# Optimization experiments

Hardware: AMD Instinct MI355X
Metric: run time of the kernel (lower is better)

## Reference

```python
import jax, jax.numpy as jnp
import numpy as np

B, H, W, C = 8, 64, 64, 256
NUM_HEADS = 8
HEAD_DIM = C // NUM_HEADS
H_SP, W_SP = 64, 8  # idx=0: h_sp=H, w_sp=split_size[1]
SCALE = HEAD_DIM ** -0.5


def img2windows(img):
    # img: [B, C, H, W] -> [B*nW, h_sp*w_sp, C]
    b, c, h, w = img.shape
    x = img.reshape(b, c, h // H_SP, H_SP, w // W_SP, W_SP)
    x = jnp.transpose(x, (0, 2, 4, 3, 5, 1))
    return x.reshape(-1, H_SP * W_SP, c)


def im2cswin(x):
    # x: [B, L, C] -> [B*nW, heads, h_sp*w_sp, head_dim]
    xi = jnp.transpose(x, (0, 2, 1)).reshape(B, C, H, W)
    xw = img2windows(xi)
    xw = xw.reshape(-1, H_SP * W_SP, NUM_HEADS, HEAD_DIM)
    return jnp.transpose(xw, (0, 2, 1, 3))


def get_lepe(x, conv_w, conv_b):
    xi = jnp.transpose(x, (0, 2, 1)).reshape(B, C, H, W)
    xi = xi.reshape(B, C, H // H_SP, H_SP, W // W_SP, W_SP)
    xi = jnp.transpose(xi, (0, 2, 4, 1, 3, 5)).reshape(-1, C, H_SP, W_SP)
    # depthwise 3x3 conv, padding 1
    lepe = jax.lax.conv_general_dilated(
        xi, conv_w, window_strides=(1, 1), padding=((1, 1), (1, 1)),
        feature_group_count=C, dimension_numbers=('NCHW', 'OIHW', 'NCHW'))
    lepe = lepe + conv_b[None, :, None, None]
    def to_heads(t):
        t = t.reshape(-1, NUM_HEADS, HEAD_DIM, H_SP * W_SP)
        return jnp.transpose(t, (0, 1, 3, 2))
    return to_heads(xi), to_heads(lepe)


def windows2img(xw):
    # xw: [B*nW, h_sp*w_sp, C] -> [B, H, W, C]
    x = xw.reshape(B, H // H_SP, W // W_SP, H_SP, W_SP, C)
    x = jnp.transpose(x, (0, 1, 3, 2, 4, 5))
    return x.reshape(B, H, W, C)


def setup_inputs() -> dict:
    key = jax.random.key(0)
    k1, k2, k3 = jax.random.split(key, 3)
    x = jax.random.normal(k1, (3, B, H * W, C), dtype=jnp.float32)
    conv_w = jax.random.normal(k2, (C, 1, 3, 3), dtype=jnp.float32) * 0.1
    conv_b = jax.random.normal(k3, (C,), dtype=jnp.float32) * 0.1
    return {"x": x, "conv_w": conv_w, "conv_b": conv_b}


def reference(x, conv_w, conv_b):
    q, k, v = x[0], x[1], x[2]
    qh = im2cswin(q) * SCALE          # [nW*B, h, S, d]
    kh = im2cswin(k)
    vh, lepe = get_lepe(v, conv_w, conv_b)
    attn = jnp.einsum('whsd,whtd->whst', qh, kh)
    attn = jax.nn.softmax(attn, axis=-1)
    out = jnp.einsum('whst,whtd->whsd', attn, vh) + lepe
    out = jnp.transpose(out, (0, 2, 1, 3)).reshape(-1, H_SP * W_SP, C)
    return windows2img(out).reshape(B, H * W, C)
```

## Files before the change

kernel.cpp:

```cpp
#include <hip/hip_runtime.h>

typedef __attribute__((ext_vector_type(8))) __bf16 bf16x8;
typedef __attribute__((ext_vector_type(4))) __bf16 bf16x4;
typedef __attribute__((ext_vector_type(4))) _Float16 half4;
typedef __attribute__((ext_vector_type(4))) float floatx4;

static __device__ __forceinline__ floatx4 mfma_qk(bf16x8 a, bf16x8 b, floatx4 c) {
    return __builtin_amdgcn_mfma_f32_16x16x32_bf16(a, b, c, 0, 0, 0);
}
static __device__ __forceinline__ floatx4 mfma_pv(half4 a, half4 b, floatx4 c) {
    return __builtin_amdgcn_mfma_f32_16x16x16f16(a, b, c, 0, 0, 0);
}

static __device__ __forceinline__ float4 gload4(const float* p) {
    float4 r;
    asm volatile("global_load_dwordx4 %0, %1, off"
                 : "=v"(r) : "v"(p) : "memory");
    return r;
}

#define QSCALE 0.25504099302278787f

__global__ __launch_bounds__(256, 2) void lepe_attn_kernel(
    const float* __restrict__ x, const float* __restrict__ conv_w,
    const float* __restrict__ conv_b, float* __restrict__ out)
{
    const int bx = blockIdx.x;
    const int wi = bx >> 4;
    const int hd = (bx >> 1) & 7;
    const int shalf = bx & 1;
    const int b = wi >> 3, wblk = wi & 7;
    const int tid = threadIdx.x;
    const int wave = tid >> 6, lane = tid & 63;
    const int g = lane >> 4, ln = lane & 15;

    __shared__ __align__(16) __bf16   Ks[2][128][32];
    __shared__ __align__(16) _Float16 VsT[32][522];
    __shared__ float Wc[32][9];
    __shared__ float Bc[32];

    const float* qp = x;
    const float* kp = x + 8 * 4096 * 256;
    const float* vp = x + 2 * 8 * 4096 * 256;
    const int base  = b * 4096 * 256;
    const int cbase = hd * 32;
    const int wcol0 = wblk * 8;
    const int qcb   = shalf * 8 + wave;

    int tP[4], fP[4], off0[4];
    #pragma unroll
    for (int p = 0; p < 4; p++) {
        int i = tid + p * 256;
        tP[p] = i >> 3; fP[p] = i & 7;
        off0[p] = base + ((tP[p] >> 3) << 14) + (wcol0 + (tP[p] & 7)) * 256
                + cbase + fP[p] * 4;
    }

    float4 kx[4], vx[4];
    #pragma unroll
    for (int p = 0; p < 4; p++) {
        kx[p] = gload4(kp + off0[p]);
        vx[p] = gload4(vp + off0[p]);
    }

    bf16x8 bq[4];
    #pragma unroll
    for (int c = 0; c < 2; c++) {
        #pragma unroll
        for (int ss = 0; ss < 2; ss++) {
            int s = (qcb + 4 * c) * 32 + ss * 16 + ln;
            int l = ((s >> 3) << 6) + wcol0 + (s & 7);
            const float* qb = qp + base + l * 256 + cbase + g * 8;
            float4 a = *(const float4*)qb, d = *(const float4*)(qb + 4);
            bf16x8 q;
            q[0] = (__bf16)(a.x * QSCALE); q[1] = (__bf16)(a.y * QSCALE);
            q[2] = (__bf16)(a.z * QSCALE); q[3] = (__bf16)(a.w * QSCALE);
            q[4] = (__bf16)(d.x * QSCALE); q[5] = (__bf16)(d.y * QSCALE);
            q[6] = (__bf16)(d.z * QSCALE); q[7] = (__bf16)(d.w * QSCALE);
            bq[c * 2 + ss] = q;
        }
    }

    asm volatile("s_waitcnt vmcnt(0)" ::: "memory");
    __builtin_amdgcn_sched_barrier(0);
    #pragma unroll
    for (int p = 0; p < 4; p++) {
        bf16x4 kk = { (__bf16)kx[p].x, (__bf16)kx[p].y,
                      (__bf16)kx[p].z, (__bf16)kx[p].w };
        *(bf16x4*)&Ks[0][tP[p]][fP[p] * 4] = kk;
        VsT[fP[p]*4+0][tP[p]] = (_Float16)vx[p].x;
        VsT[fP[p]*4+1][tP[p]] = (_Float16)vx[p].y;
        VsT[fP[p]*4+2][tP[p]] = (_Float16)vx[p].z;
        VsT[fP[p]*4+3][tP[p]] = (_Float16)vx[p].w;
    }
    for (int i = tid; i < 288; i += 256)
        Wc[i / 9][i % 9] = conv_w[(cbase + i / 9) * 9 + (i % 9)];
    if (tid < 32) Bc[tid] = conv_b[cbase + tid];
    __syncthreads();

    floatx4 aLo[4], aHi[4], aSum[4];
    #pragma unroll
    for (int u = 0; u < 4; u++) {
        aLo[u]  = (floatx4){0.f,0.f,0.f,0.f};
        aHi[u]  = (floatx4){0.f,0.f,0.f,0.f};
        aSum[u] = (floatx4){0.f,0.f,0.f,0.f};
    }
    const floatx4 zf = {0.f,0.f,0.f,0.f};
    const half4 ones = {(_Float16)1.f,(_Float16)1.f,(_Float16)1.f,(_Float16)1.f};

    auto compute_tile = [&](int j) {
        const __bf16 (*KT)[32] = Ks[j & 1];
        #pragma unroll 4
        for (int tl = 0; tl < 8; tl++) {
            bf16x8 ak = *(const bf16x8*)&KT[tl * 16 + ln][g * 8];
            int tcol = j * 128 + tl * 16 + g * 4;
            const unsigned* r0 = (const unsigned*)&VsT[ln][0];
            const unsigned* r1 = (const unsigned*)&VsT[16 + ln][0];
            half4 av0, av1;
            ((unsigned*)&av0)[0] = r0[tcol >> 1];
            ((unsigned*)&av0)[1] = r0[(tcol >> 1) + 1];
            ((unsigned*)&av1)[0] = r1[tcol >> 1];
            ((unsigned*)&av1)[1] = r1[(tcol >> 1) + 1];
            #pragma unroll
            for (int u = 0; u < 4; u++) {
                floatx4 sc = mfma_qk(ak, bq[u], zf);
                half4 ph;
                #pragma unroll
                for (int r = 0; r < 4; r++)
                    ph[r] = (_Float16)__builtin_amdgcn_exp2f(sc[r]);
                aLo[u]  = mfma_pv(av0, ph, aLo[u]);
                aHi[u]  = mfma_pv(av1, ph, aHi[u]);
                aSum[u] = mfma_pv(ones, ph, aSum[u]);
            }
        }
    };

    for (int j = 0; j < 3; j++) {
        #pragma unroll
        for (int p = 0; p < 4; p++) {
            const float* kq = kp + off0[p] + (j + 1) * 262144;
            const float* vq = vp + off0[p] + (j + 1) * 262144;
            kx[p] = gload4(kq);
            vx[p] = gload4(vq);
        }

        __builtin_amdgcn_s_setprio(1);
        compute_tile(j);
        __builtin_amdgcn_s_setprio(0);

        asm volatile("s_waitcnt vmcnt(0)" ::: "memory");
        __builtin_amdgcn_sched_barrier(0);
        #pragma unroll
        for (int p = 0; p < 4; p++) {
            bf16x4 kk = { (__bf16)kx[p].x, (__bf16)kx[p].y,
                          (__bf16)kx[p].z, (__bf16)kx[p].w };
            *(bf16x4*)&Ks[(j + 1) & 1][tP[p]][fP[p] * 4] = kk;
            int tg = 128 * (j + 1) + tP[p];
            VsT[fP[p]*4+0][tg] = (_Float16)vx[p].x;
            VsT[fP[p]*4+1][tg] = (_Float16)vx[p].y;
            VsT[fP[p]*4+2][tg] = (_Float16)vx[p].z;
            VsT[fP[p]*4+3][tg] = (_Float16)vx[p].w;
        }
        __syncthreads();
    }
    __builtin_amdgcn_s_setprio(1);
    compute_tile(3);
    __builtin_amdgcn_s_setprio(0);

    float inv[4];
    #pragma unroll
    for (int u = 0; u < 4; u++)
        inv[u] = 1.0f / aSum[u][0];

    #pragma unroll
    for (int c = 0; c < 2; c++) {
        #pragma unroll
        for (int ss = 0; ss < 2; ss++) {
            int u = c * 2 + ss;
            int s = (qcb + 4 * c) * 32 + ss * 16 + ln;
            int h = s >> 3, w = s & 7;
            int l = h * 64 + wcol0 + w;
            floatx4 alo = aLo[u], ahi = aHi[u];
            float4 olo, ohi;
            #pragma unroll
            for (int r = 0; r < 4; r++) {
                int ddl = g * 4 + r;
                float lepl = Bc[ddl];
                float leph = Bc[16 + ddl];
                #pragma unroll
                for (int ky = 0; ky < 3; ky++) {
                    int hh = h + ky - 1;
                    bool okh = (hh >= 0) & (hh < 64);
                    #pragma unroll
                    for (int kx2 = 0; kx2 < 3; kx2++) {
                        int ww = w + kx2 - 1;
                        bool ok = okh & (ww >= 0) & (ww < 8);
                        float vl = ok ? (float)VsT[ddl][hh * 8 + ww] : 0.f;
                        float vh = ok ? (float)VsT[16 + ddl][hh * 8 + ww] : 0.f;
                        lepl = fmaf(vl, Wc[ddl][ky * 3 + kx2], lepl);
                        leph = fmaf(vh, Wc[16 + ddl][ky * 3 + kx2], leph);
                    }
                }
                ((float*)&olo)[r] = alo[r] * inv[u] + lepl;
                ((float*)&ohi)[r] = ahi[r] * inv[u] + leph;
            }
            float* ob = out + base + l * 256 + cbase;
            *(float4*)(ob + g * 4) = olo;
            *(float4*)(ob + 16 + g * 4) = ohi;
        }
    }
}

extern "C" void kernel_launch(void* const* d_in, const int* in_sizes, int n_in,
                              void* d_out, int out_size, void* d_ws, size_t ws_size,
                              hipStream_t stream) {
    const float* x  = (const float*)d_in[0];
    const float* cw = (const float*)d_in[1];
    const float* cb = (const float*)d_in[2];
    float* out = (float*)d_out;
    lepe_attn_kernel<<<dim3(1024), dim3(256), 0, stream>>>(x, cw, cb, out);
}
```

Measured before the change: 192.8 us.

## Process full window per block and load all K/V up front

Each block now handles all 512 queries of a window-head instead of half, so the grid drops from 1024 to 512 blocks and each K/V tile is staged once per window-head rather than twice. The double-buffered per-tile K/V pipeline is replaced by issuing all 32 global loads at once and draining them in order with staged vmcnt waits into a single full-size K buffer, followed by one compute loop. This halves redundant K/V global traffic and conversion work but doubles accumulator and Q registers per thread and removes load/compute overlap, which can hurt occupancy under launch_bounds(256,2). With only 512 blocks, device fill may also suffer.

Result: no change. 196.3 us (+1.8%).

```diff
diff --git a/kernel.cpp b/kernel.cpp
--- a/kernel.cpp
+++ b/kernel.cpp
@@ -26,15 +26,13 @@
     const float* __restrict__ conv_b, float* __restrict__ out)
 {
     const int bx = blockIdx.x;
-    const int wi = bx >> 4;
-    const int hd = (bx >> 1) & 7;
-    const int shalf = bx & 1;
+    const int wi = bx >> 3, hd = bx & 7;
     const int b = wi >> 3, wblk = wi & 7;
     const int tid = threadIdx.x;
     const int wave = tid >> 6, lane = tid & 63;
     const int g = lane >> 4, ln = lane & 15;
 
-    __shared__ __align__(16) __bf16   Ks[2][128][32];
+    __shared__ __align__(16) __bf16   Ks[512][32];
     __shared__ __align__(16) _Float16 VsT[32][522];
     __shared__ float Wc[32][9];
     __shared__ float Bc[32];
@@ -45,30 +43,17 @@
     const int base  = b * 4096 * 256;
     const int cbase = hd * 32;
     const int wcol0 = wblk * 8;
-    const int qcb   = shalf * 8 + wave;
 
-    int tP[4], fP[4], off0[4];
+    const int f  = tid & 7, t0 = tid >> 3;
+    const int off0 = base + (((t0 >> 3) << 6) + wcol0 + (t0 & 7)) * 256
+                   + cbase + f * 4;
+
+    bf16x8 bq[8];
     #pragma unroll
-    for (int p = 0; p < 4; p++) {
-        int i = tid + p * 256;
-        tP[p] = i >> 3; fP[p] = i & 7;
-        off0[p] = base + ((tP[p] >> 3) << 14) + (wcol0 + (tP[p] & 7)) * 256
-                + cbase + fP[p] * 4;
-    }
-
-    float4 kx[4], vx[4];
-    #pragma unroll
-    for (int p = 0; p < 4; p++) {
-        kx[p] = gload4(kp + off0[p]);
-        vx[p] = gload4(vp + off0[p]);
-    }
-
-    bf16x8 bq[4];
-    #pragma unroll
-    for (int c = 0; c < 2; c++) {
+    for (int c = 0; c < 4; c++) {
         #pragma unroll
         for (int ss = 0; ss < 2; ss++) {
-            int s = (qcb + 4 * c) * 32 + ss * 16 + ln;
+            int s = (wave + 4 * c) * 32 + ss * 16 + ln;
             int l = ((s >> 3) << 6) + wcol0 + (s & 7);
             const float* qb = qp + base + l * 256 + cbase + g * 8;
             float4 a = *(const float4*)qb, d = *(const float4*)(qb + 4);
@@ -81,26 +66,43 @@
         }
     }
 
-    asm volatile("s_waitcnt vmcnt(0)" ::: "memory");
-    __builtin_amdgcn_sched_barrier(0);
-    #pragma unroll
-    for (int p = 0; p < 4; p++) {
-        bf16x4 kk = { (__bf16)kx[p].x, (__bf16)kx[p].y,
-                      (__bf16)kx[p].z, (__bf16)kx[p].w };
-        *(bf16x4*)&Ks[0][tP[p]][fP[p] * 4] = kk;
-        VsT[fP[p]*4+0][tP[p]] = (_Float16)vx[p].x;
-        VsT[fP[p]*4+1][tP[p]] = (_Float16)vx[p].y;
-        VsT[fP[p]*4+2][tP[p]] = (_Float16)vx[p].z;
-        VsT[fP[p]*4+3][tP[p]] = (_Float16)vx[p].w;
-    }
     for (int i = tid; i < 288; i += 256)
         Wc[i / 9][i % 9] = conv_w[(cbase + i / 9) * 9 + (i % 9)];
     if (tid < 32) Bc[tid] = conv_b[cbase + tid];
+
+    __builtin_amdgcn_sched_barrier(0);
+
+    float4 kx[16], vx[16];
+    #pragma unroll
+    for (int it = 0; it < 16; it++) {
+        kx[it] = gload4(kp + off0 + it * 65536);
+        vx[it] = gload4(vp + off0 + it * 65536);
+    }
+
+#define DRAIN_PAIR(IT, CNT) do {                                           \
+        asm volatile("s_waitcnt vmcnt(" #CNT ")" ::: "memory");            \
+        __builtin_amdgcn_sched_barrier(0);                                 \
+        int t = t0 + (IT) * 32;                                            \
+        bf16x4 kk = { (__bf16)kx[IT].x, (__bf16)kx[IT].y,                  \
+                      (__bf16)kx[IT].z, (__bf16)kx[IT].w };                \
+        *(bf16x4*)&Ks[t][f * 4] = kk;                                      \
+        VsT[f*4+0][t] = (_Float16)vx[IT].x;                                \
+        VsT[f*4+1][t] = (_Float16)vx[IT].y;                                \
+        VsT[f*4+2][t] = (_Float16)vx[IT].z;                                \
+        VsT[f*4+3][t] = (_Float16)vx[IT].w;                                \
+    } while (0)
+
+    DRAIN_PAIR(0, 30);  DRAIN_PAIR(1, 28);  DRAIN_PAIR(2, 26);  DRAIN_PAIR(3, 24);
+    DRAIN_PAIR(4, 22);  DRAIN_PAIR(5, 20);  DRAIN_PAIR(6, 18);  DRAIN_PAIR(7, 16);
+    DRAIN_PAIR(8, 14);  DRAIN_PAIR(9, 12);  DRAIN_PAIR(10, 10); DRAIN_PAIR(11, 8);
+    DRAIN_PAIR(12, 6);  DRAIN_PAIR(13, 4);  DRAIN_PAIR(14, 2);  DRAIN_PAIR(15, 0);
+#undef DRAIN_PAIR
+
     __syncthreads();
 
-    floatx4 aLo[4], aHi[4], aSum[4];
+    floatx4 aLo[8], aHi[8], aSum[8];
     #pragma unroll
-    for (int u = 0; u < 4; u++) {
+    for (int u = 0; u < 8; u++) {
         aLo[u]  = (floatx4){0.f,0.f,0.f,0.f};
         aHi[u]  = (floatx4){0.f,0.f,0.f,0.f};
         aSum[u] = (floatx4){0.f,0.f,0.f,0.f};
@@ -108,76 +110,41 @@
     const floatx4 zf = {0.f,0.f,0.f,0.f};
     const half4 ones = {(_Float16)1.f,(_Float16)1.f,(_Float16)1.f,(_Float16)1.f};
 
-    auto compute_tile = [&](int j) {
-        const __bf16 (*KT)[32] = Ks[j & 1];
-        #pragma unroll 4
-        for (int tl = 0; tl < 8; tl++) {
-            bf16x8 ak = *(const bf16x8*)&KT[tl * 16 + ln][g * 8];
-            int tcol = j * 128 + tl * 16 + g * 4;
-            const unsigned* r0 = (const unsigned*)&VsT[ln][0];
-            const unsigned* r1 = (const unsigned*)&VsT[16 + ln][0];
-            half4 av0, av1;
-            ((unsigned*)&av0)[0] = r0[tcol >> 1];
-            ((unsigned*)&av0)[1] = r0[(tcol >> 1) + 1];
-            ((unsigned*)&av1)[0] = r1[tcol >> 1];
-            ((unsigned*)&av1)[1] = r1[(tcol >> 1) + 1];
+    #pragma unroll 2
+    for (int tb = 0; tb < 32; tb++) {
+        bf16x8 ak = *(const bf16x8*)&Ks[tb * 16 + ln][g * 8];
+        int tcol = tb * 16 + g * 4;
+        const unsigned* r0 = (const unsigned*)&VsT[ln][0];
+        const unsigned* r1 = (const unsigned*)&VsT[16 + ln][0];
+        half4 av0, av1;
+        ((unsigned*)&av0)[0] = r0[tcol >> 1];
+        ((unsigned*)&av0)[1] = r0[(tcol >> 1) + 1];
+        ((unsigned*)&av1)[0] = r1[tcol >> 1];
+        ((unsigned*)&av1)[1] = r1[(tcol >> 1) + 1];
+        #pragma unroll
+        for (int u = 0; u < 8; u++) {
+            floatx4 sc = mfma_qk(ak, bq[u], zf);
+            half4 ph;
             #pragma unroll
-            for (int u = 0; u < 4; u++) {
-                floatx4 sc = mfma_qk(ak, bq[u], zf);
-                half4 ph;
-                #pragma unroll
-                for (int r = 0; r < 4; r++)
-                    ph[r] = (_Float16)__builtin_amdgcn_exp2f(sc[r]);
-                aLo[u]  = mfma_pv(av0, ph, aLo[u]);
-                aHi[u]  = mfma_pv(av1, ph, aHi[u]);
-                aSum[u] = mfma_pv(ones, ph, aSum[u]);
-            }
+            for (int r = 0; r < 4; r++)
+                ph[r] = (_Float16)__builtin_amdgcn_exp2f(sc[r]);
+            aLo[u]  = mfma_pv(av0, ph, aLo[u]);
+            aHi[u]  = mfma_pv(av1, ph, aHi[u]);
+            aSum[u] = mfma_pv(ones, ph, aSum[u]);
         }
-    };
+    }
 
-    for (int j = 0; j < 3; j++) {
-        #pragma unroll
-        for (int p = 0; p < 4; p++) {
-            const float* kq = kp + off0[p] + (j + 1) * 262144;
-            const float* vq = vp + off0[p] + (j + 1) * 262144;
-            kx[p] = gload4(kq);
-            vx[p] = gload4(vq);
-        }
-
-        __builtin_amdgcn_s_setprio(1);
-        compute_tile(j);
-        __builtin_amdgcn_s_setprio(0);
-
-        asm volatile("s_waitcnt vmcnt(0)" ::: "memory");
-        __builtin_amdgcn_sched_barrier(0);
-        #pragma unroll
-        for (int p = 0; p < 4; p++) {
-            bf16x4 kk = { (__bf16)kx[p].x, (__bf16)kx[p].y,
-                          (__bf16)kx[p].z, (__bf16)kx[p].w };
-            *(bf16x4*)&Ks[(j + 1) & 1][tP[p]][fP[p] * 4] = kk;
-            int tg = 128 * (j + 1) + tP[p];
-            VsT[fP[p]*4+0][tg] = (_Float16)vx[p].x;
-            VsT[fP[p]*4+1][tg] = (_Float16)vx[p].y;
-            VsT[fP[p]*4+2][tg] = (_Float16)vx[p].z;
-            VsT[fP[p]*4+3][tg] = (_Float16)vx[p].w;
-        }
-        __syncthreads();
-    }
-    __builtin_amdgcn_s_setprio(1);
-    compute_tile(3);
-    __builtin_amdgcn_s_setprio(0);
-
-    float inv[4];
+    float inv[8];
     #pragma unroll
-    for (int u = 0; u < 4; u++)
+    for (int u = 0; u < 8; u++)
         inv[u] = 1.0f / aSum[u][0];
 
     #pragma unroll
-    for (int c = 0; c < 2; c++) {
+    for (int c = 0; c < 4; c++) {
         #pragma unroll
         for (int ss = 0; ss < 2; ss++) {
             int u = c * 2 + ss;
-            int s = (qcb + 4 * c) * 32 + ss * 16 + ln;
+            int s = (wave + 4 * c) * 32 + ss * 16 + ln;
             int h = s >> 3, w = s & 7;
             int l = h * 64 + wcol0 + w;
             floatx4 alo = aLo[u], ahi = aHi[u];
@@ -218,5 +185,5 @@
     const float* cw = (const float*)d_in[1];
     const float* cb = (const float*)d_in[2];
     float* out = (float*)d_out;
-    lepe_attn_kernel<<<dim3(1024), dim3(256), 0, stream>>>(x, cw, cb, out);
+    lepe_attn_kernel<<<dim3(512), dim3(256), 0, stream>>>(x, cw, cb, out);
 }
```
